# Optimization experiments

Hardware: AMD Instinct MI355X
Metric: run time of the kernel (lower is better)

Reference implementation:

```python
import jax, jax.numpy as jnp
import numpy as np

NUM_VIEWS = 6
NUM_HEADS = 16
NUM_LAYERS = 2
DIST_THRESHOLD = 10.0
EPS = 1e-5


def layer_norm(x, g, b):
    m = jnp.mean(x, axis=-1, keepdims=True)
    v = jnp.mean((x - m) ** 2, axis=-1, keepdims=True)
    return (x - m) / jnp.sqrt(v + EPS) * g + b


def build_mask(coords3d, num_views, threshold):
    # coords3d: (B, T, 3) -> bool mask (B, T, T), True = masked
    B, T, _ = coords3d.shape
    tpv = T // num_views
    c = jnp.nan_to_num(coords3d, nan=0.0, posinf=100.0, neginf=-100.0)
    view_ids = jnp.repeat(jnp.arange(num_views), tpv)
    same_view = view_ids[:, None] == view_ids[None, :]  # (T, T)
    dist_sq = jnp.sum((c[:, :, None, :] - c[:, None, :, :]) ** 2, axis=-1)  # (B,T,T)
    mask = same_view[None] | (dist_sq > threshold * threshold)
    all_masked = jnp.all(mask, axis=-1)  # (B, T)
    eye = jnp.eye(T, dtype=bool)
    # unmask diagonal for rows that are fully masked (matches torch fix)
    mask = jnp.where(all_masked[:, :, None] & eye[None], False, mask)
    return mask


def mha(x, qkv_w, qkv_b, out_w, out_b, mask, num_heads):
    # x: (B,T,C); qkv_w: (3C,C); out_w: (C,C); mask: (B,T,T) True=masked
    B, T, C = x.shape
    hd = C // num_heads
    qkv = x @ qkv_w.T + qkv_b  # (B,T,3C)
    q, k, v = jnp.split(qkv, 3, axis=-1)
    def heads(t):
        return t.reshape(B, T, num_heads, hd).transpose(0, 2, 1, 3)  # (B,H,T,hd)
    q, k, v = heads(q), heads(k), heads(v)
    scale = 1.0 / jnp.sqrt(jnp.asarray(hd, x.dtype))
    scores = jnp.einsum('bhqd,bhkd->bhqk', q * scale, k)
    scores = jnp.where(mask[:, None], -jnp.inf, scores)
    attn = jax.nn.softmax(scores, axis=-1)
    o = jnp.einsum('bhqk,bhkd->bhqd', attn, v)  # (B,H,T,hd)
    o = o.transpose(0, 2, 1, 3).reshape(B, T, C)
    return o @ out_w.T + out_b


def setup_inputs() -> dict:
    key = jax.random.key(0)
    B, T, C, L = 2, 1536, 1024, NUM_LAYERS
    ks = jax.random.split(key, 16)
    s = 0.02
    inp = {
        'pos_embed': jax.random.normal(ks[0], (B, T, C), jnp.float32),
        'coords3d': jax.random.normal(ks[1], (B, T, 3), jnp.float32) * 8.0,
        'ln1_g': jnp.ones((L, C), jnp.float32),
        'ln1_b': jnp.zeros((L, C), jnp.float32),
        'qkv_w': jax.random.normal(ks[2], (L, 3 * C, C), jnp.float32) * s,
        'qkv_b': jnp.zeros((L, 3 * C), jnp.float32),
        'out_w': jax.random.normal(ks[3], (L, C, C), jnp.float32) * s,
        'out_b': jnp.zeros((L, C), jnp.float32),
        'ln2_g': jnp.ones((L, C), jnp.float32),
        'ln2_b': jnp.zeros((L, C), jnp.float32),
        'ffn_w1': jax.random.normal(ks[4], (L, 4 * C, C), jnp.float32) * s,
        'ffn_b1': jnp.zeros((L, 4 * C), jnp.float32),
        'ffn_w2': jax.random.normal(ks[5], (L, C, 4 * C), jnp.float32) * s,
        'ffn_b2': jnp.zeros((L, C), jnp.float32),
        'norm_g': jnp.ones((C,), jnp.float32),
        'norm_b': jnp.zeros((C,), jnp.float32),
    }
    return inp


def reference(pos_embed, coords3d, ln1_g, ln1_b, qkv_w, qkv_b, out_w, out_b,
              ln2_g, ln2_b, ffn_w1, ffn_b1, ffn_w2, ffn_b2, norm_g, norm_b):
    mask = build_mask(coords3d, NUM_VIEWS, DIST_THRESHOLD)
    x = pos_embed
    for l in range(NUM_LAYERS):
        xn = layer_norm(x, ln1_g[l], ln1_b[l])
        x = x + mha(xn, qkv_w[l], qkv_b[l], out_w[l], out_b[l], mask, NUM_HEADS)
        xn = layer_norm(x, ln2_g[l], ln2_b[l])
        h = jax.nn.gelu(xn @ ffn_w1[l].T + ffn_b1[l], approximate=False)
        x = x + (h @ ffn_w2[l].T + ffn_b2[l])
    return layer_norm(x, norm_g, norm_b)
```

## Files before the change

kernel.cpp:

```cpp
#include <hip/hip_runtime.h>

#define TT 1536
#define CC 1024
#define NH 16
#define HD 64
#define NL 2
#define NB 2
#define MM (NB*TT)

typedef unsigned short u16;
typedef unsigned int u32;
typedef unsigned long long u64;
typedef __attribute__((ext_vector_type(8))) short short8v;
typedef __attribute__((ext_vector_type(4))) float f32x4;

__device__ __forceinline__ u16 f2bf(float f){
  u32 u = __float_as_uint(f);
  u32 r = (u + 0x7FFFu + ((u >> 16) & 1u)) >> 16;
  return (u16)r;
}

__device__ __forceinline__ void gload_lds16(const void* g, void* l){
  __builtin_amdgcn_global_load_lds(
      (const __attribute__((address_space(1))) void*)g,
      (__attribute__((address_space(3))) void*)l, 16, 0, 0);
}

__device__ __forceinline__ f32x4 mfma16(short8v a, short8v b, f32x4 c){
  return __builtin_amdgcn_mfma_f32_16x16x32_bf16(a, b, c, 0, 0, 0);
}

__device__ __forceinline__ float exp2f_fast(float x){
  return __builtin_amdgcn_exp2f(x);
}

__device__ __forceinline__ u32 cvt_pk_bf16(float lo, float hi){
  u32 r;
  asm("v_cvt_pk_bf16_f32 %0, %1, %2" : "=v"(r) : "v"(lo), "v"(hi));
  return r;
}

__global__ __launch_bounds__(256) void cvt_bf16_kernel(const float* __restrict__ in,
                                                       u16* __restrict__ out, int n4){
  int stride = gridDim.x * 256;
  for (int i = blockIdx.x * 256 + threadIdx.x; i < n4; i += stride){
    const float4 v = ((const float4*)in)[i];
    ushort4 o;
    o.x = f2bf(v.x); o.y = f2bf(v.y); o.z = f2bf(v.z); o.w = f2bf(v.w);
    ((ushort4*)out)[i] = o;
  }
}

__device__ __forceinline__ float fixc(float v){
  if (__builtin_isnan(v)) return 0.0f;
  if (__builtin_isinf(v)) return v > 0.0f ? 100.0f : -100.0f;
  return v;
}

__global__ __launch_bounds__(256) void mask_kernel(const float* __restrict__ coords,
                                                   u64* __restrict__ maskw){
  const int tid = threadIdx.x, wave = tid >> 6, lane = tid & 63;
  const int ri = blockIdx.x * 4 + wave;
  const int b = ri / TT, i = ri - b * TT;
  const float* cp = coords + (size_t)ri * 3;
  const float cx = fixc(cp[0]), cy = fixc(cp[1]), cz = fixc(cp[2]);
  const int vi = i >> 8;
  u64 allm = ~0ull;
  for (int ch = 0; ch < 24; ++ch){
    const int j = ch * 64 + lane;
    const float* cj = coords + ((size_t)b * TT + j) * 3;
    const float dx = cx - fixc(cj[0]);
    const float dy = cy - fixc(cj[1]);
    const float dz = cz - fixc(cj[2]);
    const float d2 = dx*dx + dy*dy + dz*dz;
    const bool masked = ((j >> 8) == vi) || (d2 > 100.0f);
    const u64 bal = __ballot(masked);
    if (lane == 0) maskw[(size_t)ri * 24 + ch] = bal;
    allm &= bal;
  }
  if (lane == 0 && allm == ~0ull){
    const size_t w = (size_t)ri * 24 + (i >> 6);
    maskw[w] &= ~(1ull << (i & 63));
  }
}

template<int OUTF>
__global__ __launch_bounds__(256) void ln_kernel(const float* __restrict__ x,
    const float* __restrict__ gw, const float* __restrict__ bw,
    u16* __restrict__ outb, float* __restrict__ outf){
  __shared__ float sred[4];
  const int tid = threadIdx.x, wave = tid >> 6, lane = tid & 63;
  const size_t row = blockIdx.x;
  const float4 v = *(const float4*)(x + row * CC + tid * 4);
  float s = v.x + v.y + v.z + v.w;
  #pragma unroll
  for (int o = 1; o < 64; o <<= 1) s += __shfl_xor(s, o, 64);
  if (lane == 0) sred[wave] = s;
  __syncthreads();
  const float mean = (sred[0] + sred[1] + sred[2] + sred[3]) * (1.0f / CC);
  __syncthreads();
  const float d0 = v.x - mean, d1 = v.y - mean, d2 = v.z - mean, d3 = v.w - mean;
  float q = d0*d0 + d1*d1 + d2*d2 + d3*d3;
  #pragma unroll
  for (int o = 1; o < 64; o <<= 1) q += __shfl_xor(q, o, 64);
  if (lane == 0) sred[wave] = q;
  __syncthreads();
  const float var = (sred[0] + sred[1] + sred[2] + sred[3]) * (1.0f / CC);
  const float rstd = rsqrtf(var + 1e-5f);
  const float4 g4 = *(const float4*)(gw + tid * 4);
  const float4 b4 = *(const float4*)(bw + tid * 4);
  const float y0 = d0 * rstd * g4.x + b4.x;
  const float y1 = d1 * rstd * g4.y + b4.y;
  const float y2 = d2 * rstd * g4.z + b4.z;
  const float y3 = d3 * rstd * g4.w + b4.w;
  if (OUTF){
    *(float4*)(outf + row * CC + tid * 4) = make_float4(y0, y1, y2, y3);
  } else {
    ushort4 o4; o4.x = f2bf(y0); o4.y = f2bf(y1); o4.z = f2bf(y2); o4.w = f2bf(y3);
    *(ushort4*)(outb + row * CC + tid * 4) = o4;
  }
}

template<int EPI, int BM>
__global__ __launch_bounds__(512, 4) void gemm_nt(const u16* __restrict__ A,
    const u16* __restrict__ Bw, const float* __restrict__ bias,
    const float* __restrict__ res, u16* __restrict__ outb, float* __restrict__ outf,
    int M, int N, int K){
  __shared__ u16 As[2][BM][64];
  __shared__ u16 Bs[2][128][64];
  const int tid = threadIdx.x, wave = tid >> 6, lane = tid & 63;
  const int gx = gridDim.x;
  const int nwg = gx * gridDim.y;
  const int orig = blockIdx.y * gx + blockIdx.x;
  const int qq = nwg >> 3, rm = nwg & 7;
  const int xcd = orig & 7, pos = orig >> 3;
  const int wg = (xcd < rm ? xcd * (qq + 1) : rm * (qq + 1) + (xcd - rm) * qq) + pos;
  const int m0 = (wg / gx) * BM, n0 = (wg % gx) * 128;
  constexpr int NFR = (BM == 128) ? 4 : 2;
  constexpr int CW = 16 * NFR;
  const int wr = (BM == 128) ? (wave >> 1) : (wave >> 2);
  const int wc = (BM == 128) ? (wave & 1) : (wave & 3);
  f32x4 acc[2][NFR];
  #pragma unroll
  for (int mi = 0; mi < 2; ++mi)
    #pragma unroll
    for (int ni = 0; ni < NFR; ++ni){ f32x4 z = {0.f,0.f,0.f,0.f}; acc[mi][ni] = z; }

  const u16* Ag = A + (size_t)m0 * K;
  const u16* Bg = Bw + (size_t)n0 * K;
  const int srow0 = wave * 8 + (lane >> 3);
  const int scole = ((lane & 7) ^ (lane >> 3)) * 8;
  auto stage = [&](int buf, int k0){
    char* ab = (char*)&As[buf][0][0];
    char* bb = (char*)&Bs[buf][0][0];
    #pragma unroll
    for (int l = 0; l < BM/64; ++l)
      gload_lds16(Ag + (size_t)(l*64 + srow0) * K + k0 + scole, ab + (l*8 + wave) * 1024);
    #pragma unroll
    for (int l = 0; l < 2; ++l)
      gload_lds16(Bg + (size_t)(l*64 + srow0) * K + k0 + scole, bb + (l*8 + wave) * 1024);
  };

  const int NT = K >> 6;
  stage(0, 0);
  stage(1, 64);

  const int ar = lane & 15, akb = (lane >> 4) * 16;
  const int rsw = (ar & 7) << 4;
  for (int t = 0; t < NT; ++t){
    const int cur = t & 1;
    if (t + 1 < NT){
      if constexpr (BM == 128) asm volatile("s_waitcnt vmcnt(4)" ::: "memory");
      else                     asm volatile("s_waitcnt vmcnt(3)" ::: "memory");
    } else {
      asm volatile("s_waitcnt vmcnt(0)" ::: "memory");
    }
    __builtin_amdgcn_s_barrier();
    const char* ab = (const char*)&As[cur][0][0];
    const char* bb = (const char*)&Bs[cur][0][0];
    short8v af[2][2], bf[NFR][2];
    #pragma unroll
    for (int ks = 0; ks < 2; ++ks){
      const int cb = (ks*64 + akb) ^ rsw;
      #pragma unroll
      for (int mi = 0; mi < 2; ++mi)
        af[mi][ks] = *(const short8v*)(ab + (wr*32 + mi*16 + ar)*128 + cb);
      #pragma unroll
      for (int ni = 0; ni < NFR; ++ni)
        bf[ni][ks] = *(const short8v*)(bb + (wc*CW + ni*16 + ar)*128 + cb);
    }
    asm volatile("s_waitcnt lgkmcnt(0)" ::: "memory");
    __builtin_amdgcn_sched_barrier(0);
    __builtin_amdgcn_s_barrier();
    if (t + 2 < NT) stage(cur, (t + 2) * 64);
    __builtin_amdgcn_s_setprio(1);
    #pragma unroll
    for (int ks = 0; ks < 2; ++ks)
      #pragma unroll
      for (int mi = 0; mi < 2; ++mi)
        #pragma unroll
        for (int ni = 0; ni < NFR; ++ni)
          acc[mi][ni] = mfma16(af[mi][ks], bf[ni][ks], acc[mi][ni]);
    __builtin_amdgcn_s_setprio(0);
  }

  const int cr = (lane >> 4) * 4, cl = lane & 15;
  #pragma unroll
  for (int ni = 0; ni < NFR; ++ni){
    const int c = n0 + wc*CW + ni*16 + cl;
    const float bv = bias[c];
    #pragma unroll
    for (int mi = 0; mi < 2; ++mi){
      #pragma unroll
      for (int r = 0; r < 4; ++r){
        const size_t rr2 = (size_t)(m0 + wr*32 + mi*16 + cr + r);
        float v = acc[mi][ni][r] + bv;
        if constexpr (EPI == 1) v = 0.5f * v * (1.0f + erff(v * 0.70710678118654752f));
        if constexpr (EPI == 2) outf[rr2 * N + c] = v + res[rr2 * N + c];
        else outb[rr2 * N + c] = f2bf(v);
      }
    }
  }
}

__global__ __launch_bounds__(256, 3) void attn_kernel(const u16* __restrict__ qkv,
    const u64* __restrict__ maskw, u16* __restrict__ outp){
  __shared__ u16 Ks[2][64][64];
  __shared__ u16 Vt[2][64][64];
  __shared__ u16 Ps[4][16][64];
  const int tid = threadIdx.x, wave = tid >> 6, lane = tid & 63;
  const int b = blockIdx.y >> 4, h = blockIdx.y & 15;
  const int qb = blockIdx.x * 64;
  const int rs = 3 * CC;
  const int g4 = lane >> 4;
  const int l15 = lane & 15;
  const int qrow = qb + wave * 16 + l15;
  const u16* kv_base = qkv + (size_t)b * TT * rs;

  const float qscale = 0.18033688011112042f;
  const u16* qp = kv_base + (size_t)qrow * rs + h * HD + g4 * 8;
  short8v qf0, qf1;
  {
    const short8v r0 = *(const short8v*)qp;
    const short8v r1 = *(const short8v*)(qp + 32);
    #pragma unroll
    for (int e = 0; e < 8; ++e){
      qf0[e] = (short)f2bf(__uint_as_float(((u32)(u16)r0[e]) << 16) * qscale);
      qf1[e] = (short)f2bf(__uint_as_float(((u32)(u16)r1[e]) << 16) * qscale);
    }
  }

  f32x4 o[4], lacc;
  #pragma unroll
  for (int dt = 0; dt < 4; ++dt){ f32x4 z = {0.f,0.f,0.f,0.f}; o[dt] = z; }
  { f32x4 z = {0.f,0.f,0.f,0.f}; lacc = z; }
  float m_r = -1.0e4f;

  const int sw = (l15 & 7) << 4;
  const int swl = (lane & 7) << 4;
  int koff[4][2], voff[4][2], pwoff[4], proff[2], vwoff[2];
  #pragma unroll
  for (int jt = 0; jt < 4; ++jt){
    koff[jt][0] = (jt*16 + l15)*128 + ((g4*16) ^ sw);
    koff[jt][1] = (jt*16 + l15)*128 + ((64 + g4*16) ^ sw);
    voff[jt][0] = koff[jt][0];
    voff[jt][1] = koff[jt][1];
    pwoff[jt] = wave*2048 + l15*128 + ((jt*32 + g4*8) ^ sw);
  }
  proff[0] = wave*2048 + l15*128 + ((g4*16) ^ sw);
  proff[1] = wave*2048 + l15*128 + ((64 + g4*16) ^ sw);
  vwoff[0] = lane*128 + ((wave*16) ^ swl);
  vwoff[1] = lane*128 + ((64 + wave*16) ^ swl);

  const int scol = CC + h * HD + (((lane & 7) ^ (lane >> 3)) * 8);
  const u16* skp0 = kv_base + (size_t)(64 + wave*16 + (lane >> 3)) * rs + scol;
  const u16* skp1 = skp0 + 8 * rs;
  const u16* vp   = kv_base + (size_t)(64 + wave*8) * rs + 2*CC + h*HD + lane;
  const u64* mp2  = maskw + (size_t)(b * TT + qrow) * 24;

  char* KsB = (char*)&Ks[0][0][0];
  char* VtB = (char*)&Vt[0][0][0];
  char* PsB = (char*)&Ps[0][0][0];

  short8v vone;
  #pragma unroll
  for (int e = 0; e < 8; ++e) vone[e] = (short)0x3F80;

  {
    u16 vv[16];
    #pragma unroll
    for (int e = 0; e < 8; ++e)
      vv[e] = kv_base[(size_t)(wave*8 + e) * rs + 2*CC + h*HD + lane];
    #pragma unroll
    for (int e = 0; e < 8; ++e)
      vv[8+e] = kv_base[(size_t)(32 + wave*8 + e) * rs + 2*CC + h*HD + lane];
    gload_lds16(kv_base + (size_t)(wave*16 + (lane>>3)) * rs + scol,
                KsB + (wave*2 + 0) * 1024);
    gload_lds16(kv_base + (size_t)(wave*16 + 8 + (lane>>3)) * rs + scol,
                KsB + (wave*2 + 1) * 1024);
    short8v sv0, sv1;
    #pragma unroll
    for (int e = 0; e < 8; ++e){ sv0[e] = (short)vv[e]; sv1[e] = (short)vv[8+e]; }
    *(short8v*)(VtB + vwoff[0]) = sv0;
    *(short8v*)(VtB + vwoff[1]) = sv1;
    __syncthreads();
  }

  auto chunk = [&](int buf, bool pf){
    u16 vv[16];
    if (pf){
      #pragma unroll
      for (int e = 0; e < 8; ++e) vv[e] = vp[(size_t)e * rs];
      #pragma unroll
      for (int e = 0; e < 8; ++e) vv[8+e] = vp[(size_t)(32 + e) * rs];
      gload_lds16(skp0, KsB + (buf^1)*8192 + (wave*2 + 0)*1024);
      gload_lds16(skp1, KsB + (buf^1)*8192 + (wave*2 + 1)*1024);
    }
    const u64 mw = mp2[buf];
    const u32 mwlo = (u32)mw, mwhi = (u32)(mw >> 32);

    const char* Kb = KsB + buf * 8192;
    f32x4 S[4];
    #pragma unroll
    for (int jt = 0; jt < 4; ++jt){
      const short8v k0 = *(const short8v*)(Kb + koff[jt][0]);
      const short8v k1 = *(const short8v*)(Kb + koff[jt][1]);
      f32x4 z = {0.f,0.f,0.f,0.f};
      z = mfma16(k0, qf0, z);
      z = mfma16(k1, qf1, z);
      S[jt] = z;
    }

    float ps[16];
    float cmax = -3.0e38f;
    #pragma unroll
    for (int jt = 0; jt < 4; ++jt){
      const u32 msrc = (jt & 2) ? mwhi : mwlo;
      const int sh = g4 * 4 + (jt & 1) * 16;
      #pragma unroll
      for (int r = 0; r < 4; ++r){
        float s = S[jt][r];
        s = ((msrc >> (sh + r)) & 1u) ? -3.0e38f : s;
        ps[jt*4+r] = s;
        cmax = fmaxf(cmax, s);
      }
    }
    cmax = fmaxf(cmax, __shfl_xor(cmax, 16));
    cmax = fmaxf(cmax, __shfl_xor(cmax, 32));

    if (!__all(cmax <= m_r + 8.0f)){
      const float mnew = fmaxf(m_r, cmax);
      const float fac = exp2f_fast(m_r - mnew);
      m_r = mnew;
      float fr4[4];
      #pragma unroll
      for (int r = 0; r < 4; ++r) fr4[r] = __shfl(fac, g4 * 4 + r);
      #pragma unroll
      for (int dt = 0; dt < 4; ++dt){
        f32x4 tt = o[dt];
        tt[0] *= fr4[0]; tt[1] *= fr4[1]; tt[2] *= fr4[2]; tt[3] *= fr4[3];
        o[dt] = tt;
      }
      lacc[0] *= fr4[0]; lacc[1] *= fr4[1]; lacc[2] *= fr4[2]; lacc[3] *= fr4[3];
    }

    #pragma unroll
    for (int i = 0; i < 16; ++i) ps[i] = exp2f_fast(ps[i] - m_r);

    #pragma unroll
    for (int jt = 0; jt < 4; ++jt){
      uint2 pk;
      pk.x = cvt_pk_bf16(ps[jt*4+0], ps[jt*4+1]);
      pk.y = cvt_pk_bf16(ps[jt*4+2], ps[jt*4+3]);
      *(uint2*)(PsB + pwoff[jt]) = pk;
    }

    short8v pA[2];
    pA[0] = *(const short8v*)(PsB + proff[0]);
    pA[1] = *(const short8v*)(PsB + proff[1]);
    const char* Vb = VtB + buf * 8192;
    __builtin_amdgcn_s_setprio(1);
    #pragma unroll
    for (int dt = 0; dt < 4; ++dt){
      #pragma unroll
      for (int kc = 0; kc < 2; ++kc){
        const short8v vf = *(const short8v*)(Vb + voff[dt][kc]);
        o[dt] = mfma16(pA[kc], vf, o[dt]);
      }
    }
    lacc = mfma16(pA[0], vone, lacc);
    lacc = mfma16(pA[1], vone, lacc);
    __builtin_amdgcn_s_setprio(0);

    if (pf){
      short8v sv0, sv1;
      #pragma unroll
      for (int e = 0; e < 8; ++e){ sv0[e] = (short)vv[e]; sv1[e] = (short)vv[8+e]; }
      char* Vd = VtB + (buf^1) * 8192;
      *(short8v*)(Vd + vwoff[0]) = sv0;
      *(short8v*)(Vd + vwoff[1]) = sv1;
      vp += (size_t)64 * rs; skp0 += (size_t)64 * rs; skp1 += (size_t)64 * rs;
    }
    __syncthreads();
  };

  for (int th = 0; th < 12; ++th){
    chunk(0, true);
    chunk(1, th < 11);
    mp2 += 2;
  }

  float linv[4];
  #pragma unroll
  for (int r = 0; r < 4; ++r) linv[r] = 1.0f / fmaxf(lacc[r], 1e-30f);
  #pragma unroll
  for (int dt = 0; dt < 4; ++dt)
    #pragma unroll
    for (int r = 0; r < 4; ++r)
      outp[(size_t)(b * TT + qb + wave * 16 + g4 * 4 + r) * CC + h * HD + dt * 16 + l15] =
          f2bf(o[dt][r] * linv[r]);
}

extern "C" void kernel_launch(void* const* d_in, const int* in_sizes, int n_in,
                              void* d_out, int out_size, void* d_ws, size_t ws_size,
                              hipStream_t stream){
  (void)in_sizes; (void)n_in; (void)out_size; (void)ws_size;
  const float* pos    = (const float*)d_in[0];
  const float* coords = (const float*)d_in[1];
  const float* ln1g   = (const float*)d_in[2];
  const float* ln1b   = (const float*)d_in[3];
  const float* qkvw   = (const float*)d_in[4];
  const float* qkvbi  = (const float*)d_in[5];
  const float* outw   = (const float*)d_in[6];
  const float* outbi  = (const float*)d_in[7];
  const float* ln2g   = (const float*)d_in[8];
  const float* ln2b   = (const float*)d_in[9];
  const float* w1     = (const float*)d_in[10];
  const float* b1     = (const float*)d_in[11];
  const float* w2     = (const float*)d_in[12];
  const float* b2     = (const float*)d_in[13];
  const float* ng     = (const float*)d_in[14];
  const float* nbb    = (const float*)d_in[15];

  char* wsp = (char*)d_ws;
  size_t off = 0;
  auto alloc = [&](size_t bytes)->void*{
    void* p = wsp + off; off += (bytes + 255) & ~(size_t)255; return p;
  };
  u16* qkvw_bf = (u16*)alloc((size_t)NL*3*CC*CC*sizeof(u16));
  u16* outw_bf = (u16*)alloc((size_t)NL*CC*CC*sizeof(u16));
  u16* w1_bf   = (u16*)alloc((size_t)NL*4*CC*CC*sizeof(u16));
  u16* w2_bf   = (u16*)alloc((size_t)NL*4*CC*CC*sizeof(u16));
  float* x     = (float*)alloc((size_t)MM*CC*sizeof(float));
  u16* xn      = (u16*)alloc((size_t)MM*CC*sizeof(u16));
  u16* qkvbuf  = (u16*)alloc((size_t)MM*4*CC*sizeof(u16));
  u16* attnb   = (u16*)alloc((size_t)MM*CC*sizeof(u16));
  u64* maskw   = (u64*)alloc((size_t)MM*24*sizeof(u64));
  u16* hbuf = qkvbuf;

  auto cvt = [&](const float* s, u16* dst, size_t n){
    int n4 = (int)(n >> 2);
    int blocks = (n4 + 255) / 256; if (blocks > 4096) blocks = 4096;
    cvt_bf16_kernel<<<dim3(blocks), dim3(256), 0, stream>>>(s, dst, n4);
  };
  cvt(qkvw, qkvw_bf, (size_t)NL*3*CC*CC);
  cvt(outw, outw_bf, (size_t)NL*CC*CC);
  cvt(w1, w1_bf, (size_t)NL*4*CC*CC);
  cvt(w2, w2_bf, (size_t)NL*4*CC*CC);

  hipMemcpyAsync(x, pos, (size_t)MM*CC*sizeof(float), hipMemcpyDeviceToDevice, stream);
  mask_kernel<<<dim3(MM/4), dim3(256), 0, stream>>>(coords, maskw);

  for (int l = 0; l < NL; ++l){
    ln_kernel<0><<<dim3(MM), dim3(256), 0, stream>>>(x, ln1g + l*CC, ln1b + l*CC, xn, nullptr);
    gemm_nt<0,128><<<dim3(3*CC/128, MM/128), dim3(512), 0, stream>>>(
        xn, qkvw_bf + (size_t)l*3*CC*CC, qkvbi + l*3*CC, nullptr, qkvbuf, nullptr, MM, 3*CC, CC);
    attn_kernel<<<dim3(TT/64, NB*NH), dim3(256), 0, stream>>>(qkvbuf, maskw, attnb);
    gemm_nt<2,64><<<dim3(CC/128, MM/64), dim3(512), 0, stream>>>(
        attnb, outw_bf + (size_t)l*CC*CC, outbi + l*CC, x, nullptr, x, MM, CC, CC);
    ln_kernel<0><<<dim3(MM), dim3(256), 0, stream>>>(x, ln2g + l*CC, ln2b + l*CC, xn, nullptr);
    gemm_nt<1,128><<<dim3(4*CC/128, MM/128), dim3(512), 0, stream>>>(
        xn, w1_bf + (size_t)l*4*CC*CC, b1 + l*4*CC, nullptr, hbuf, nullptr, MM, 4*CC, CC);
    gemm_nt<2,64><<<dim3(CC/128, MM/64), dim3(512), 0, stream>>>(
        hbuf, w2_bf + (size_t)l*4*CC*CC, b2 + l*CC, x, nullptr, x, MM, CC, 4*CC);
  }
  ln_kernel<1><<<dim3(MM), dim3(256), 0, stream>>>(x, ng, nbb, nullptr, (float*)d_out);
}
```

Baseline: 432.4 us.

## Rewrite GEMM with 64x64 per-wave tiles, fewer threads, single-buffered BK=32

Restructures the GEMM kernel so each wave computes a 64x64 output tile with 4x4 MFMA fragments, using 128 or 256 threads per block instead of 512. The K loop now stages 32-wide slices into a single LDS buffer with plain syncthreads, dropping the double-buffered prefetch, swizzled layout and priority hints. This aims to raise per-wave register reuse of loaded fragments but loses load/compute overlap and may introduce LDS bank conflicts.

```diff
diff --git a/kernel.cpp b/kernel.cpp
--- a/kernel.cpp
+++ b/kernel.cpp
@@ -122,12 +122,14 @@
 }
 
 template<int EPI, int BM>
-__global__ __launch_bounds__(512, 4) void gemm_nt(const u16* __restrict__ A,
+__global__ __launch_bounds__(BM*2) void gemm_nt(const u16* __restrict__ A,
     const u16* __restrict__ Bw, const float* __restrict__ bias,
     const float* __restrict__ res, u16* __restrict__ outb, float* __restrict__ outf,
     int M, int N, int K){
-  __shared__ u16 As[2][BM][64];
-  __shared__ u16 Bs[2][128][64];
+  constexpr int NT = BM * 2;
+  constexpr int CB = 8192 / (NT * 16);
+  __shared__ u16 As[BM][32];
+  __shared__ u16 Bs[128][32];
   const int tid = threadIdx.x, wave = tid >> 6, lane = tid & 63;
   const int gx = gridDim.x;
   const int nwg = gx * gridDim.y;
@@ -136,84 +138,55 @@
   const int xcd = orig & 7, pos = orig >> 3;
   const int wg = (xcd < rm ? xcd * (qq + 1) : rm * (qq + 1) + (xcd - rm) * qq) + pos;
   const int m0 = (wg / gx) * BM, n0 = (wg % gx) * 128;
-  constexpr int NFR = (BM == 128) ? 4 : 2;
-  constexpr int CW = 16 * NFR;
-  const int wr = (BM == 128) ? (wave >> 1) : (wave >> 2);
-  const int wc = (BM == 128) ? (wave & 1) : (wave & 3);
-  f32x4 acc[2][NFR];
-  #pragma unroll
-  for (int mi = 0; mi < 2; ++mi)
-    #pragma unroll
-    for (int ni = 0; ni < NFR; ++ni){ f32x4 z = {0.f,0.f,0.f,0.f}; acc[mi][ni] = z; }
+  const int wr = wave >> 1, wc = wave & 1;
+  f32x4 acc[4][4];
+  #pragma unroll
+  for (int mi = 0; mi < 4; ++mi)
+    #pragma unroll
+    for (int ni = 0; ni < 4; ++ni){ f32x4 z = {0.f,0.f,0.f,0.f}; acc[mi][ni] = z; }
 
   const u16* Ag = A + (size_t)m0 * K;
   const u16* Bg = Bw + (size_t)n0 * K;
-  const int srow0 = wave * 8 + (lane >> 3);
-  const int scole = ((lane & 7) ^ (lane >> 3)) * 8;
-  auto stage = [&](int buf, int k0){
-    char* ab = (char*)&As[buf][0][0];
-    char* bb = (char*)&Bs[buf][0][0];
-    #pragma unroll
-    for (int l = 0; l < BM/64; ++l)
-      gload_lds16(Ag + (size_t)(l*64 + srow0) * K + k0 + scole, ab + (l*8 + wave) * 1024);
-    #pragma unroll
-    for (int l = 0; l < 2; ++l)
-      gload_lds16(Bg + (size_t)(l*64 + srow0) * K + k0 + scole, bb + (l*8 + wave) * 1024);
-  };
-
-  const int NT = K >> 6;
-  stage(0, 0);
-  stage(1, 64);
-
-  const int ar = lane & 15, akb = (lane >> 4) * 16;
-  const int rsw = (ar & 7) << 4;
-  for (int t = 0; t < NT; ++t){
-    const int cur = t & 1;
-    if (t + 1 < NT){
-      if constexpr (BM == 128) asm volatile("s_waitcnt vmcnt(4)" ::: "memory");
-      else                     asm volatile("s_waitcnt vmcnt(3)" ::: "memory");
-    } else {
-      asm volatile("s_waitcnt vmcnt(0)" ::: "memory");
-    }
-    __builtin_amdgcn_s_barrier();
-    const char* ab = (const char*)&As[cur][0][0];
-    const char* bb = (const char*)&Bs[cur][0][0];
-    short8v af[2][2], bf[NFR][2];
-    #pragma unroll
-    for (int ks = 0; ks < 2; ++ks){
-      const int cb = (ks*64 + akb) ^ rsw;
-      #pragma unroll
-      for (int mi = 0; mi < 2; ++mi)
-        af[mi][ks] = *(const short8v*)(ab + (wr*32 + mi*16 + ar)*128 + cb);
-      #pragma unroll
-      for (int ni = 0; ni < NFR; ++ni)
-        bf[ni][ks] = *(const short8v*)(bb + (wc*CW + ni*16 + ar)*128 + cb);
-    }
-    asm volatile("s_waitcnt lgkmcnt(0)" ::: "memory");
-    __builtin_amdgcn_sched_barrier(0);
-    __builtin_amdgcn_s_barrier();
-    if (t + 2 < NT) stage(cur, (t + 2) * 64);
-    __builtin_amdgcn_s_setprio(1);
-    #pragma unroll
-    for (int ks = 0; ks < 2; ++ks)
-      #pragma unroll
-      for (int mi = 0; mi < 2; ++mi)
-        #pragma unroll
-        for (int ni = 0; ni < NFR; ++ni)
-          acc[mi][ni] = mfma16(af[mi][ks], bf[ni][ks], acc[mi][ni]);
-    __builtin_amdgcn_s_setprio(0);
-  }
-
-  const int cr = (lane >> 4) * 4, cl = lane & 15;
-  #pragma unroll
-  for (int ni = 0; ni < NFR; ++ni){
-    const int c = n0 + wc*CW + ni*16 + cl;
+  const int srow = tid >> 2;
+  const int scol = (tid & 3) * 8;
+  const int l15 = lane & 15, g4 = lane >> 4;
+  char* const ab0 = (char*)&As[0][0];
+  char* const bb0 = (char*)&Bs[0][0];
+
+  for (int k0 = 0; k0 < K; k0 += 32){
+    #pragma unroll
+    for (int c = 0; c < 2; ++c)
+      gload_lds16(Ag + (size_t)(c*(NT/4) + srow) * K + k0 + scol,
+                  ab0 + c*(NT*16) + tid*16);
+    #pragma unroll
+    for (int c = 0; c < CB; ++c)
+      gload_lds16(Bg + (size_t)(c*(NT/4) + srow) * K + k0 + scol,
+                  bb0 + c*(NT*16) + tid*16);
+    __syncthreads();
+    short8v af[4], bf[4];
+    #pragma unroll
+    for (int t = 0; t < 4; ++t){
+      af[t] = *(const short8v*)(ab0 + (wr*64 + t*16 + l15)*64 + g4*16);
+      bf[t] = *(const short8v*)(bb0 + (wc*64 + t*16 + l15)*64 + g4*16);
+    }
+    #pragma unroll
+    for (int mi = 0; mi < 4; ++mi)
+      #pragma unroll
+      for (int ni = 0; ni < 4; ++ni)
+        acc[mi][ni] = mfma16(af[mi], bf[ni], acc[mi][ni]);
+    __syncthreads();
+  }
+
+  const int cr = g4 * 4, cl = l15;
+  #pragma unroll
+  for (int ni = 0; ni < 4; ++ni){
+    const int c = n0 + wc*64 + ni*16 + cl;
     const float bv = bias[c];
     #pragma unroll
-    for (int mi = 0; mi < 2; ++mi){
+    for (int mi = 0; mi < 4; ++mi){
       #pragma unroll
       for (int r = 0; r < 4; ++r){
-        const size_t rr2 = (size_t)(m0 + wr*32 + mi*16 + cr + r);
+        const size_t rr2 = (size_t)(m0 + wr*64 + mi*16 + cr + r);
         float v = acc[mi][ni][r] + bv;
         if constexpr (EPI == 1) v = 0.5f * v * (1.0f + erff(v * 0.70710678118654752f));
         if constexpr (EPI == 2) outf[rr2 * N + c] = v + res[rr2 * N + c];
@@ -473,15 +446,15 @@
 
   for (int l = 0; l < NL; ++l){
     ln_kernel<0><<<dim3(MM), dim3(256), 0, stream>>>(x, ln1g + l*CC, ln1b + l*CC, xn, nullptr);
-    gemm_nt<0,128><<<dim3(3*CC/128, MM/128), dim3(512), 0, stream>>>(
+    gemm_nt<0,128><<<dim3(3*CC/128, MM/128), dim3(256), 0, stream>>>(
         xn, qkvw_bf + (size_t)l*3*CC*CC, qkvbi + l*3*CC, nullptr, qkvbuf, nullptr, MM, 3*CC, CC);
     attn_kernel<<<dim3(TT/64, NB*NH), dim3(256), 0, stream>>>(qkvbuf, maskw, attnb);
-    gemm_nt<2,64><<<dim3(CC/128, MM/64), dim3(512), 0, stream>>>(
+    gemm_nt<2,64><<<dim3(CC/128, MM/64), dim3(128), 0, stream>>>(
         attnb, outw_bf + (size_t)l*CC*CC, outbi + l*CC, x, nullptr, x, MM, CC, CC);
     ln_kernel<0><<<dim3(MM), dim3(256), 0, stream>>>(x, ln2g + l*CC, ln2b + l*CC, xn, nullptr);
-    gemm_nt<1,128><<<dim3(4*CC/128, MM/128), dim3(512), 0, stream>>>(
+    gemm_nt<1,128><<<dim3(4*CC/128, MM/128), dim3(256), 0, stream>>>(
         xn, w1_bf + (size_t)l*4*CC*CC, b1 + l*4*CC, nullptr, hbuf, nullptr, MM, 4*CC, CC);
-    gemm_nt<2,64><<<dim3(CC/128, MM/64), dim3(512), 0, stream>>>(
+    gemm_nt<2,64><<<dim3(CC/128, MM/64), dim3(128), 0, stream>>>(
         hbuf, w2_bf + (size_t)l*4*CC*CC, b2 + l*CC, x, nullptr, x, MM, CC, 4*CC);
   }
   ln_kernel<1><<<dim3(MM), dim3(256), 0, stream>>>(x, ng, nbb, nullptr, (float*)d_out);
```

Measured after the change: 581.2 us. +34.4%, slower.
